# Kernel optimization log

Hardware: AMD Instinct MI355X
Metric: run time of the kernel (lower is better)

Reference implementation:

```python
import jax, jax.numpy as jnp
import numpy as np

B, S, D, H, DFF = 4, 2048, 1024, 16, 4096
DK = D // H  # = d_v
NEG = -1e30  # stands in for float('-inf'); fully-masked rows zeroed explicitly


def setup_inputs() -> dict:
    key = jax.random.key(0)
    ks = jax.random.split(key, 12)
    scale = lambda fan_in: fan_in ** -0.5
    # padding mask: positions >= random length are padded (True = pad)
    lens = jax.random.randint(ks[0], (B,), S // 2, S + 1)
    src_padding_mask = jnp.arange(S)[None, :] >= lens[:, None]
    return {
        "src": jax.random.normal(ks[1], (B, S, D), jnp.float32),
        "src_padding_mask": src_padding_mask,
        # per-head projections, stored as [H, D, DK] (x @ W, i.e. torch W.T)
        "Wq": jax.random.normal(ks[2], (H, D, DK), jnp.float32) * scale(D),
        "Wk": jax.random.normal(ks[3], (H, D, DK), jnp.float32) * scale(D),
        "Wv": jax.random.normal(ks[4], (H, D, DK), jnp.float32) * scale(D),
        "Wo": jax.random.normal(ks[5], (D, D), jnp.float32) * scale(D),
        "g1": jnp.ones((D,), jnp.float32),
        "g2": jnp.ones((D,), jnp.float32),
        "W1": jax.random.normal(ks[6], (D, DFF), jnp.float32) * scale(D),
        "V1": jax.random.normal(ks[7], (D, DFF), jnp.float32) * scale(D),
        "W2": jax.random.normal(ks[8], (DFF, D), jnp.float32) * scale(DFF),
    }


def _rmsnorm(x, gamma):
    # rms = sqrt(sum(x^2)/size); out = gamma * x / rms
    rms = jnp.sqrt(jnp.sum(x * x, axis=-1, keepdims=True) / x.shape[-1])
    return gamma * x / rms


def _encoder_layer(src, pad_mask, Wq, Wk, Wv, Wo, g1, g2, W1, V1, W2):
    x = _rmsnorm(src, g1)
    # all heads at once: q,k,v -> [B,H,S,DK]
    q = jnp.einsum('bsd,hdk->bhsk', x, Wq)
    k = jnp.einsum('bsd,hdk->bhsk', x, Wk)
    v = jnp.einsum('bsd,hdk->bhsk', x, Wv)
    scores = jnp.einsum('bhsk,bhtk->bhst', q, k) * (DK ** -0.5)  # [B,H,S,S]
    mask = pad_mask[:, None, :, None] | pad_mask[:, None, None, :]
    scores = jnp.where(mask, NEG, scores)
    attn = jax.nn.softmax(scores, axis=-1)
    # torch: fully -inf rows softmax to nan -> nan_to_num(0). Zero padded query rows.
    attn = jnp.where(pad_mask[:, None, :, None], 0.0, attn)
    o = jnp.einsum('bhst,bhtk->bhsk', attn, v)            # [B,H,S,DK]
    o = o.transpose(0, 2, 1, 3).reshape(src.shape[0], src.shape[1], -1)  # concat heads
    sa = src + o @ Wo
    y = _rmsnorm(sa, g2)
    ff = (jax.nn.silu(y @ W1) * (y @ V1)) @ W2
    return sa + ff


def reference(src, src_padding_mask, Wq, Wk, Wv, Wo, g1, g2, W1, V1, W2):
    return _encoder_layer(src, src_padding_mask, Wq, Wk, Wv, Wo, g1, g2, W1, V1, W2)
```

## Files before the change

### kernel.cpp

```cpp
#include <hip/hip_runtime.h>
#include <hip/hip_bf16.h>

typedef short short8 __attribute__((ext_vector_type(8)));
typedef float f32x4 __attribute__((ext_vector_type(4)));
typedef float f32x16 __attribute__((ext_vector_type(16)));
typedef unsigned short u16;
typedef unsigned short u16x4 __attribute__((ext_vector_type(4)));

__device__ __forceinline__ u16 f2bf(float f) {
  __hip_bfloat16 h = __float2bfloat16(f);
  return __builtin_bit_cast(u16, h);
}
__device__ __forceinline__ float bf2f(u16 u) {
  return __bfloat162float(__builtin_bit_cast(__hip_bfloat16, u));
}
__device__ __forceinline__ void gload_lds16(const void* g, void* l) {
  __builtin_amdgcn_global_load_lds(
      (const __attribute__((address_space(1))) void*)g,
      (__attribute__((address_space(3))) void*)l, 16, 0, 0);
}
__device__ __forceinline__ unsigned cvtpk(float lo, float hi) {
  unsigned r;
  asm("v_cvt_pk_bf16_f32 %0, %1, %2" : "=v"(r) : "v"(lo), "v"(hi));
  return r;
}

__global__ void compute_lens(const unsigned char* __restrict__ mask, int* __restrict__ lens) {
  __shared__ int flag;
  __shared__ int cnt[4];
  const int tid = threadIdx.x;
  if (tid == 0) flag = 0;
  if (tid < 4) cnt[tid] = 0;
  __syncthreads();
  int found = 0;
  for (int i = tid; i < 8192; i += 256)
    if (mask[i] == 1 && (i & 3) != 0) found = 1;
  if (found) atomicOr(&flag, 1);
  __syncthreads();
  int l0 = 0, l1 = 0, l2 = 0, l3 = 0;
  if (flag) {
    for (int i = tid; i < 8192; i += 256) {
      int z = (mask[i] == 0);
      int b = i >> 11;
      l0 += z & (b == 0); l1 += z & (b == 1); l2 += z & (b == 2); l3 += z & (b == 3);
    }
  } else {
    const int* mi = (const int*)mask;
    for (int i = tid; i < 8192; i += 256) {
      int z = (mi[i] == 0);
      int b = i >> 11;
      l0 += z & (b == 0); l1 += z & (b == 1); l2 += z & (b == 2); l3 += z & (b == 3);
    }
  }
  if (l0) atomicAdd(&cnt[0], l0);
  if (l1) atomicAdd(&cnt[1], l1);
  if (l2) atomicAdd(&cnt[2], l2);
  if (l3) atomicAdd(&cnt[3], l3);
  __syncthreads();
  if (tid < 4) lens[tid] = cnt[tid];
}

__global__ void convT(const float* __restrict__ in, u16* __restrict__ out,
                      int K, int N, long inz, long outz, int ilv) {
  __shared__ float t[32][33];
  const int n0 = blockIdx.x * 32, k0 = blockIdx.y * 32;
  const float* ip = in + (size_t)blockIdx.z * inz;
  u16* op = out + (size_t)blockIdx.z * outz;
  const int tx = threadIdx.x & 31, ty = threadIdx.x >> 5;
  for (int i = ty; i < 32; i += 8)
    t[i][tx] = ip[(size_t)(k0 + i) * N + n0 + tx];
  __syncthreads();
  for (int i = ty; i < 32; i += 8) {
    const int rn = n0 + i;
    const int r = ilv ? ((((rn >> 4) << 5) | (rn & 15)) | ((ilv - 1) << 4)) : rn;
    op[(size_t)r * K + k0 + tx] = f2bf(t[tx][i]);
  }
}

__global__ void rmsnorm_kernel(const float* __restrict__ in, const float* __restrict__ g,
                               u16* __restrict__ out) {
  __shared__ float psum[4];
  const int row = blockIdx.x, tid = threadIdx.x;
  const float4 x = ((const float4*)(in + (size_t)row * 1024))[tid];
  float ss = x.x * x.x + x.y * x.y + x.z * x.z + x.w * x.w;
  for (int m = 1; m < 64; m <<= 1) ss += __shfl_xor(ss, m, 64);
  if ((tid & 63) == 0) psum[tid >> 6] = ss;
  __syncthreads();
  const float tot = psum[0] + psum[1] + psum[2] + psum[3];
  const float inv = rsqrtf(tot * (1.0f / 1024.0f));
  const float4 gv = ((const float4*)g)[tid];
  u16x4 o;
  o[0] = f2bf(gv.x * x.x * inv); o[1] = f2bf(gv.y * x.y * inv);
  o[2] = f2bf(gv.z * x.z * inv); o[3] = f2bf(gv.w * x.w * inv);
  *(u16x4*)&out[(size_t)row * 1024 + tid * 4] = o;
}

enum { MQKV = 0, MSA = 1, MFSILU = 2, MFF2 = 3 };

template <int MODE, int BM>
__global__ __launch_bounds__(512, 2) void gemm3(
    const u16* __restrict__ A, const u16* __restrict__ Bt,
    const int K,
    u16* __restrict__ oq, u16* __restrict__ ok, u16* __restrict__ ov,
    float* __restrict__ of, const float* __restrict__ afp,
    u16* __restrict__ ob) {
  constexpr int ABUF = BM * 64;
  constexpr bool P4 = (BM == 256);
  constexpr int MR = BM / 32;
  __shared__ u16 lds[2 * ABUF + 32768];
  const int tid = threadIdx.x;
  const int w = tid >> 6, l = tid & 63;
  const int wr = w >> 2, wc = w & 3;
  const int lane16 = l & 15, lgrp = l >> 4;

  const int bid = (int)blockIdx.x, xcd = bid & 7, seq = bid >> 3;
  int by, bx;
  if (MODE == MQKV) {
    const int j = seq / 24, t5 = seq % 24;
    by = (xcd >> 2) * 16 + j * 8 + t5 / 3;
    bx = (xcd & 3) * 3 + t5 % 3;
  } else if (MODE == MFSILU) {
    by = (seq >> 5) * 8 + ((seq & 31) >> 2);
    bx = xcd * 4 + (seq & 3);
  } else {
    by = (xcd >> 1) * 16 + (seq >> 4) * 8 + ((seq & 15) >> 1);
    bx = (xcd & 1) * 2 + (seq & 1);
  }
  const int row0 = by * BM, col0 = bx * 256;

  auto stageA = [&](int kt, int buf) {
#pragma unroll
    for (int i = 0; i < BM / 64; ++i) {
      const int c = i * 512 + tid;
      const int r = c >> 3, j = (c & 7) ^ (r & 7);
      gload_lds16(A + (size_t)(row0 + r) * K + kt * 64 + j * 8,
                  &lds[buf * ABUF + c * 8]);
    }
  };
  auto stageB = [&](int kt, int buf) {
#pragma unroll
    for (int i = 0; i < 4; ++i) {
      const int c = i * 512 + tid;
      const int r = c >> 3, j = (c & 7) ^ (r & 7);
      gload_lds16(Bt + (size_t)(col0 + r) * K + kt * 64 + j * 8,
                  &lds[2 * ABUF + buf * 16384 + c * 8]);
    }
  };
  auto frofs = [&](int rrow, int ks) {
    return rrow * 64 + ((((ks << 2) + lgrp) ^ (rrow & 7)) << 3);
  };

  f32x4 zero = {0.f, 0.f, 0.f, 0.f};
  f32x4 acc[MR][4];
#pragma unroll
  for (int i = 0; i < MR; ++i)
#pragma unroll
    for (int j = 0; j < 4; ++j) acc[i][j] = zero;

  const int nkt = K >> 6;
  stageA(0, 0); stageB(0, 0); stageA(1, 1);
  if (P4) stageB(1, 1);

  for (int t = 0; t < nkt; ++t) {
    const int c = t & 1;
    if (t == nkt - 1)  asm volatile("s_waitcnt vmcnt(0)\ns_barrier" ::: "memory");
    else if (P4)       asm volatile("s_waitcnt vmcnt(8)\ns_barrier" ::: "memory");
    else               asm volatile("s_waitcnt vmcnt(2)\ns_barrier" ::: "memory");
    const u16* ap = &lds[c * ABUF];
    const u16* bp = &lds[2 * ABUF + c * 16384];
    short8 a[4][2], b01[2][2], b23[2][2];

    if (!P4) { if (t + 1 < nkt) stageB(t + 1, c ^ 1); }
#pragma unroll
    for (int mi = 0; mi < 4; ++mi)
#pragma unroll
      for (int ks = 0; ks < 2; ++ks)
        a[mi][ks] = *(const short8*)&ap[frofs(wr * (BM / 2) + mi * 16 + lane16, ks)];
#pragma unroll
    for (int ni = 0; ni < 2; ++ni)
#pragma unroll
      for (int ks = 0; ks < 2; ++ks) {
        b01[ni][ks] = *(const short8*)&bp[frofs(wc * 64 + ni * 16 + lane16, ks)];
        b23[ni][ks] = *(const short8*)&bp[frofs(wc * 64 + (ni + 2) * 16 + lane16, ks)];
      }
    __builtin_amdgcn_s_setprio(1);
#pragma unroll
    for (int ks = 0; ks < 2; ++ks)
#pragma unroll
      for (int mi = 0; mi < 4; ++mi)
#pragma unroll
        for (int ni = 0; ni < 2; ++ni)
          acc[mi][ni] = __builtin_amdgcn_mfma_f32_16x16x32_bf16(a[mi][ks], b01[ni][ks], acc[mi][ni], 0, 0, 0);
    __builtin_amdgcn_s_setprio(0);
    asm volatile("s_barrier" ::: "memory");

    if (P4) {
      __builtin_amdgcn_s_setprio(1);
#pragma unroll
      for (int ks = 0; ks < 2; ++ks)
#pragma unroll
        for (int mi = 0; mi < 4; ++mi)
#pragma unroll
          for (int ni = 0; ni < 2; ++ni)
            acc[mi][ni + 2] = __builtin_amdgcn_mfma_f32_16x16x32_bf16(a[mi][ks], b23[ni][ks], acc[mi][ni + 2], 0, 0, 0);
      __builtin_amdgcn_s_setprio(0);
#pragma unroll
      for (int mi = 0; mi < 4; ++mi)
#pragma unroll
        for (int ks = 0; ks < 2; ++ks)
          a[mi][ks] = *(const short8*)&ap[frofs(wr * 128 + (mi + 4) * 16 + lane16, ks)];
      asm volatile("s_barrier" ::: "memory");

      if (t + 2 < nkt) stageB(t + 2, c);
      __builtin_amdgcn_s_setprio(1);
#pragma unroll
      for (int ks = 0; ks < 2; ++ks)
#pragma unroll
        for (int mi = 0; mi < 4; ++mi)
#pragma unroll
          for (int ni = 0; ni < 2; ++ni)
            acc[(MR == 8 ? mi + 4 : mi)][ni] = __builtin_amdgcn_mfma_f32_16x16x32_bf16(a[mi][ks], b01[ni][ks], acc[(MR == 8 ? mi + 4 : mi)][ni], 0, 0, 0);
      __builtin_amdgcn_s_setprio(0);
      asm volatile("s_barrier" ::: "memory");

      if (t + 2 < nkt) stageA(t + 2, c);
      __builtin_amdgcn_s_setprio(1);
#pragma unroll
      for (int ks = 0; ks < 2; ++ks)
#pragma unroll
        for (int mi = 0; mi < 4; ++mi)
#pragma unroll
          for (int ni = 0; ni < 2; ++ni)
            acc[(MR == 8 ? mi + 4 : mi)][ni + 2] = __builtin_amdgcn_mfma_f32_16x16x32_bf16(a[mi][ks], b23[ni][ks], acc[(MR == 8 ? mi + 4 : mi)][ni + 2], 0, 0, 0);
      __builtin_amdgcn_s_setprio(0);
    } else {
      if (t + 2 < nkt) stageA(t + 2, c);
      __builtin_amdgcn_s_setprio(1);
#pragma unroll
      for (int ks = 0; ks < 2; ++ks)
#pragma unroll
        for (int mi = 0; mi < 4; ++mi)
#pragma unroll
          for (int ni = 0; ni < 2; ++ni)
            acc[mi][ni + 2] = __builtin_amdgcn_mfma_f32_16x16x32_bf16(a[mi][ks], b23[ni][ks], acc[mi][ni + 2], 0, 0, 0);
      __builtin_amdgcn_s_setprio(0);
    }
  }
  asm volatile("s_barrier" ::: "memory");

  if (MODE == MQKV) {
#pragma unroll
    for (int mi = 0; mi < MR; ++mi) {
      const int sbase = row0 + wr * (BM / 2) + mi * 16 + lgrp * 4;
      const int bbt = sbase >> 11, sr = sbase & 2047;
#pragma unroll
      for (int ni = 0; ni < 4; ++ni) {
        const int j = col0 + wc * 64 + ni * 16 + lane16;
        const int which = j >> 10, rr = j & 1023, h = rr >> 6, kk = rr & 63;
        const int bh = bbt * 16 + h;
        if (which == 2) {
          u16x4 pk;
#pragma unroll
          for (int r = 0; r < 4; ++r) pk[r] = f2bf(acc[mi][ni][r]);
          *(u16x4*)&ov[((size_t)bh * 64 + kk) * 2048 + sr] = pk;
        } else {
          u16* dst = (which == 0) ? oq : ok;
          const float scl = (which == 0) ? 0.125f : 1.0f;
#pragma unroll
          for (int r = 0; r < 4; ++r)
            dst[((size_t)bh * 2048 + sr + r) * 64 + kk] = f2bf(acc[mi][ni][r] * scl);
        }
      }
    }
  } else if (MODE == MFSILU) {
    u16* ep = &lds[w * 576];
    const int orow = l >> 2, ocol = (l & 3) * 8;
#pragma unroll
    for (int mi = 0; mi < MR; ++mi) {
#pragma unroll
      for (int p = 0; p < 2; ++p)
#pragma unroll
        for (int r = 0; r < 4; ++r) {
          const float h1 = acc[mi][2 * p][r], h2 = acc[mi][2 * p + 1][r];
          ep[(lgrp * 4 + r) * 34 + p * 16 + lane16] = f2bf(h1 / (1.0f + __expf(-h1)) * h2);
        }
      short8 v = *(const short8*)&ep[orow * 34 + ocol];
      *(short8*)&ob[(size_t)(row0 + wr * (BM / 2) + mi * 16 + orow) * 4096 +
                    (col0 >> 1) + wc * 32 + ocol] = v;
    }
  } else {
#pragma unroll
    for (int mi = 0; mi < MR; ++mi) {
      const int row = row0 + wr * (BM / 2) + mi * 16 + lgrp * 4;
#pragma unroll
      for (int ni = 0; ni < 4; ++ni) {
        const int j = col0 + wc * 64 + ni * 16 + lane16;
#pragma unroll
        for (int r = 0; r < 4; ++r) {
          const size_t idx = (size_t)(row + r) * 1024 + j;
          const float base = (MODE == MSA) ? afp[idx] : of[idx];
          of[idx] = base + acc[mi][ni][r];
        }
      }
    }
  }
}

__global__ void attn2_kernel(const u16* __restrict__ qb, const u16* __restrict__ kb,
                             const u16* __restrict__ vT, u16* __restrict__ obuf,
                             const int* __restrict__ lens) {
  __shared__ u16 sm[9216];
  const int tid = threadIdx.x;
  const int l = tid & 63, wid = tid >> 6;
  const int l31 = l & 31, hi = l >> 5;
  const int bh = blockIdx.x, b = bh >> 4, h = bh & 15;
  const int q0 = blockIdx.y * 128;
  const int len = lens[b];

  if (q0 >= len) {
    short8 z = {0, 0, 0, 0, 0, 0, 0, 0};
#pragma unroll
    for (int c = 0; c < 4; ++c) {
      const int ck = c * 256 + tid;
      const int r = ck >> 3, j = ck & 7;
      *(short8*)&obuf[((size_t)b * 2048 + q0 + r) * 1024 + h * 64 + j * 8] = z;
    }
    return;
  }

  const int q0w = q0 + wid * 32;
  const u16* qp = qb + ((size_t)bh * 2048 + q0w + l31) * 64;
  short8 qf0 = *(const short8*)(qp + hi * 8);
  short8 qf1 = *(const short8*)(qp + 16 + hi * 8);
  short8 qf2 = *(const short8*)(qp + 32 + hi * 8);
  short8 qf3 = *(const short8*)(qp + 48 + hi * 8);

  f32x16 oa0 = {0.f,0.f,0.f,0.f,0.f,0.f,0.f,0.f,0.f,0.f,0.f,0.f,0.f,0.f,0.f,0.f};
  f32x16 oa1 = oa0;
  float m_run = -1e30f, l_run = 0.f;

  const int swz = (l31 & 7) << 3;
  const int nt = (len + 63) >> 6;
  for (int kt = 0; kt < nt; ++kt) {
    const int t0 = kt * 64;
    __syncthreads();
#pragma unroll
    for (int c = 0; c < 2; ++c) {
      const int ck = c * 256 + wid * 64 + l;
      const int r = ck >> 3;
      const int j = (ck & 7) ^ (r & 7);
      gload_lds16(kb + ((size_t)bh * 2048 + t0 + r) * 64 + j * 8,
                  &sm[(c * 256 + wid * 64) * 8]);
      gload_lds16(vT + ((size_t)bh * 64 + r) * 2048 + t0 + j * 8,
                  &sm[4096 + (c * 256 + wid * 64) * 8]);
    }
    __syncthreads();

    f32x16 sc0 = {0.f,0.f,0.f,0.f,0.f,0.f,0.f,0.f,0.f,0.f,0.f,0.f,0.f,0.f,0.f,0.f};
    f32x16 sc1 = sc0;
#pragma unroll
    for (int ds = 0; ds < 4; ++ds) {
      const int col = (ds * 16 + hi * 8) ^ swz;
      const short8 kf0 = *(const short8*)&sm[(0 + l31) * 64 + col];
      const short8 kf1 = *(const short8*)&sm[(32 + l31) * 64 + col];
      const short8 qf = (ds == 0) ? qf0 : (ds == 1) ? qf1 : (ds == 2) ? qf2 : qf3;
      sc0 = __builtin_amdgcn_mfma_f32_32x32x16_bf16(kf0, qf, sc0, 0, 0, 0);
      sc1 = __builtin_amdgcn_mfma_f32_32x32x16_bf16(kf1, qf, sc1, 0, 0, 0);
    }

    if (t0 + 64 > len) {
      const int tb = t0 + 4 * hi;
#pragma unroll
      for (int i = 0; i < 16; ++i) {
        const int tg = tb + (i & 3) + 8 * (i >> 2);
        if (tg >= len) sc0[i] = -1e30f;
        if (tg + 32 >= len) sc1[i] = -1e30f;
      }
    }

    float mt = sc0[0];
#pragma unroll
    for (int i = 1; i < 16; ++i) mt = fmaxf(mt, sc0[i]);
#pragma unroll
    for (int i = 0; i < 16; ++i) mt = fmaxf(mt, sc1[i]);
    mt = fmaxf(mt, __shfl_xor(mt, 32, 64));
    const float mnew = fmaxf(m_run, mt);
    const float fac = __expf(m_run - mnew);
    m_run = mnew;
    float sum = 0.f;
#pragma unroll
    for (int i = 0; i < 16; ++i) { sc0[i] = __expf(sc0[i] - mnew); sum += sc0[i]; }
#pragma unroll
    for (int i = 0; i < 16; ++i) { sc1[i] = __expf(sc1[i] - mnew); sum += sc1[i]; }
    sum += __shfl_xor(sum, 32, 64);
    l_run = l_run * fac + sum;
#pragma unroll
    for (int i = 0; i < 16; ++i) { oa0[i] *= fac; oa1[i] *= fac; }

    unsigned wv[16];
#pragma unroll
    for (int k = 0; k < 8; ++k) wv[k] = cvtpk(sc0[2 * k], sc0[2 * k + 1]);
#pragma unroll
    for (int k = 0; k < 8; ++k) wv[8 + k] = cvtpk(sc1[2 * k], sc1[2 * k + 1]);
    unsigned pw[16];
#pragma unroll
    for (int s = 0; s < 2; ++s) {
#pragma unroll
      for (int half = 0; half < 2; ++half) {
        const unsigned a0 = wv[8 * s + 4 * half + 0], a1 = wv[8 * s + 4 * half + 1];
        const unsigned a2 = wv[8 * s + 4 * half + 2], a3 = wv[8 * s + 4 * half + 3];
        const unsigned e0 = (unsigned)__shfl_xor((int)(hi ? a0 : a2), 32, 64);
        const unsigned e1 = (unsigned)__shfl_xor((int)(hi ? a1 : a3), 32, 64);
        const int o = s * 8 + half * 4;
        pw[o + 0] = hi ? e0 : a0;
        pw[o + 1] = hi ? e1 : a1;
        pw[o + 2] = hi ? a2 : e0;
        pw[o + 3] = hi ? a3 : e1;
      }
    }
#pragma unroll
    for (int g = 0; g < 4; ++g) {
      union { unsigned u[4]; short8 s8; } pk;
      pk.u[0] = pw[4 * g + 0]; pk.u[1] = pw[4 * g + 1];
      pk.u[2] = pw[4 * g + 2]; pk.u[3] = pw[4 * g + 3];
      const int col = (g * 16 + hi * 8) ^ swz;
      const short8 vf0 = *(const short8*)&sm[4096 + (0 + l31) * 64 + col];
      const short8 vf1 = *(const short8*)&sm[4096 + (32 + l31) * 64 + col];
      oa0 = __builtin_amdgcn_mfma_f32_32x32x16_bf16(vf0, pk.s8, oa0, 0, 0, 0);
      oa1 = __builtin_amdgcn_mfma_f32_32x32x16_bf16(vf1, pk.s8, oa1, 0, 0, 0);
    }
  }

  __syncthreads();
  const float invl = 1.0f / l_run;
  u16* ow = &sm[wid * 2304];
#pragma unroll
  for (int i = 0; i < 16; ++i) {
    const int d0 = (i & 3) + 8 * (i >> 2) + 4 * hi;
    ow[l31 * 72 + d0] = f2bf(oa0[i] * invl);
    ow[l31 * 72 + 32 + d0] = f2bf(oa1[i] * invl);
  }
  short8 z = {0, 0, 0, 0, 0, 0, 0, 0};
#pragma unroll
  for (int c = 0; c < 4; ++c) {
    const int ck = c * 64 + l;
    const int r = ck >> 3, j = ck & 7;
    short8 v = *(const short8*)&ow[r * 72 + j * 8];
    if (q0w + r >= len) v = z;
    *(short8*)&obuf[((size_t)b * 2048 + q0w + r) * 1024 + h * 64 + j * 8] = v;
  }
}

extern "C" void kernel_launch(void* const* d_in, const int* in_sizes, int n_in,
                              void* d_out, int out_size, void* d_ws, size_t ws_size,
                              hipStream_t stream) {
  const float* src = (const float*)d_in[0];
  const unsigned char* mask = (const unsigned char*)d_in[1];
  const float* Wq = (const float*)d_in[2];
  const float* Wk = (const float*)d_in[3];
  const float* Wv = (const float*)d_in[4];
  const float* Wo = (const float*)d_in[5];
  const float* g1 = (const float*)d_in[6];
  const float* g2 = (const float*)d_in[7];
  const float* W1 = (const float*)d_in[8];
  const float* V1 = (const float*)d_in[9];
  const float* W2 = (const float*)d_in[10];
  float* out = (float*)d_out;
  char* ws = (char*)d_ws;

  int* lens   = (int*)ws;
  u16* WqkvT  = (u16*)(ws + 256);
  u16* WoT    = (u16*)(ws + 6291712);
  u16* W1V1T  = (u16*)(ws + 8388864);
  u16* W2T    = (u16*)(ws + 25166080);
  u16* xb     = (u16*)(ws + 33554688);
  u16* qbf    = (u16*)(ws + 50331904);
  u16* kbf    = (u16*)(ws + 67109120);
  u16* vTb    = (u16*)(ws + 83886336);
  u16* obf    = (u16*)(ws + 100663552);
  u16* c1     = qbf;

  compute_lens<<<1, 256, 0, stream>>>(mask, lens);
  convT<<<dim3(2, 32, 16), 256, 0, stream>>>(Wq, WqkvT, 1024, 64, 65536, 65536, 0);
  convT<<<dim3(2, 32, 16), 256, 0, stream>>>(Wk, WqkvT + 1024 * 1024, 1024, 64, 65536, 65536, 0);
  convT<<<dim3(2, 32, 16), 256, 0, stream>>>(Wv, WqkvT + 2048 * 1024, 1024, 64, 65536, 65536, 0);
  convT<<<dim3(32, 32, 1), 256, 0, stream>>>(Wo, WoT, 1024, 1024, 0, 0, 0);
  convT<<<dim3(128, 32, 1), 256, 0, stream>>>(W1, W1V1T, 1024, 4096, 0, 0, 1);
  convT<<<dim3(128, 32, 1), 256, 0, stream>>>(V1, W1V1T, 1024, 4096, 0, 0, 2);
  convT<<<dim3(32, 128, 1), 256, 0, stream>>>(W2, W2T, 4096, 1024, 0, 0, 0);

  rmsnorm_kernel<<<8192, 256, 0, stream>>>(src, g1, xb);
  gemm3<MQKV, 256><<<384, 512, 0, stream>>>(xb, WqkvT, 1024,
                                            qbf, kbf, vTb, nullptr, nullptr, nullptr);
  attn2_kernel<<<dim3(64, 16), 256, 0, stream>>>(qbf, kbf, vTb, obf, lens);
  gemm3<MSA, 128><<<256, 512, 0, stream>>>(obf, WoT, 1024,
                                           nullptr, nullptr, nullptr, out, src, nullptr);
  rmsnorm_kernel<<<8192, 256, 0, stream>>>(out, g2, xb);
  gemm3<MFSILU, 256><<<1024, 512, 0, stream>>>(xb, W1V1T, 1024,
                                               nullptr, nullptr, nullptr, nullptr, nullptr, c1);
  gemm3<MFF2, 128><<<256, 512, 0, stream>>>(c1, W2T, 4096,
                                            nullptr, nullptr, nullptr, out, nullptr, nullptr);
}
```

Before: 463.1 us.

## Restructure GEMM K-loop pipeline with split prefetch and double A fragments

Reworks the software pipeline of the bf16 MFMA GEMM. Both A and B tiles for stage t+2 are now prefetched in split halves interleaved between MFMA phases, and the vmcnt wait moves to the end of each iteration. In the 256-row variant, the second A half and the b23 fragments are loaded into separate registers ahead of the MFMAs so the LDS reads overlap compute. This costs more VGPRs and extra barriers, which at launch bounds (512,2) risks spills or lost occupancy.

```diff
diff --git a/kernel.cpp b/kernel.cpp
--- a/kernel.cpp
+++ b/kernel.cpp
@@ -107,6 +107,7 @@
   constexpr int ABUF = BM * 64;
   constexpr bool P4 = (BM == 256);
   constexpr int MR = BM / 32;
+  constexpr int AIT = BM / 64;
   __shared__ u16 lds[2 * ABUF + 32768];
   const int tid = threadIdx.x;
   const int w = tid >> 6, l = tid & 63;
@@ -128,22 +129,22 @@
   }
   const int row0 = by * BM, col0 = bx * 256;
 
-  auto stageA = [&](int kt, int buf) {
-#pragma unroll
-    for (int i = 0; i < BM / 64; ++i) {
-      const int c = i * 512 + tid;
-      const int r = c >> 3, j = (c & 7) ^ (r & 7);
+  auto stageAr = [&](int kt, int buf, int i0, int i1) {
+#pragma unroll
+    for (int i = i0; i < i1; ++i) {
+      const int cc = i * 512 + tid;
+      const int r = cc >> 3, j = (cc & 7) ^ (r & 7);
       gload_lds16(A + (size_t)(row0 + r) * K + kt * 64 + j * 8,
-                  &lds[buf * ABUF + c * 8]);
+                  &lds[buf * ABUF + cc * 8]);
     }
   };
-  auto stageB = [&](int kt, int buf) {
-#pragma unroll
-    for (int i = 0; i < 4; ++i) {
-      const int c = i * 512 + tid;
-      const int r = c >> 3, j = (c & 7) ^ (r & 7);
+  auto stageBr = [&](int kt, int buf, int i0, int i1) {
+#pragma unroll
+    for (int i = i0; i < i1; ++i) {
+      const int cc = i * 512 + tid;
+      const int r = cc >> 3, j = (cc & 7) ^ (r & 7);
       gload_lds16(Bt + (size_t)(col0 + r) * K + kt * 64 + j * 8,
-                  &lds[2 * ABUF + buf * 16384 + c * 8]);
+                  &lds[2 * ABUF + buf * 16384 + cc * 8]);
     }
   };
   auto frofs = [&](int rrow, int ks) {
@@ -158,19 +159,19 @@
     for (int j = 0; j < 4; ++j) acc[i][j] = zero;
 
   const int nkt = K >> 6;
-  stageA(0, 0); stageB(0, 0); stageA(1, 1);
-  if (P4) stageB(1, 1);
+  stageAr(0, 0, 0, AIT); stageBr(0, 0, 0, 4);
+  stageAr(1, 1, 0, AIT); stageBr(1, 1, 0, 4);
+  if (P4) asm volatile("s_waitcnt vmcnt(8)" ::: "memory");
+  else    asm volatile("s_waitcnt vmcnt(6)" ::: "memory");
+  __builtin_amdgcn_s_barrier();
 
   for (int t = 0; t < nkt; ++t) {
     const int c = t & 1;
-    if (t == nkt - 1)  asm volatile("s_waitcnt vmcnt(0)\ns_barrier" ::: "memory");
-    else if (P4)       asm volatile("s_waitcnt vmcnt(8)\ns_barrier" ::: "memory");
-    else               asm volatile("s_waitcnt vmcnt(2)\ns_barrier" ::: "memory");
+    const bool pf = (t + 2 < nkt);
     const u16* ap = &lds[c * ABUF];
     const u16* bp = &lds[2 * ABUF + c * 16384];
-    short8 a[4][2], b01[2][2], b23[2][2];
-
-    if (!P4) { if (t + 1 < nkt) stageB(t + 1, c ^ 1); }
+    short8 a[4][2], a2[4][2], b01[2][2], b23[2][2];
+
 #pragma unroll
     for (int mi = 0; mi < 4; ++mi)
 #pragma unroll
@@ -179,10 +180,17 @@
 #pragma unroll
     for (int ni = 0; ni < 2; ++ni)
 #pragma unroll
-      for (int ks = 0; ks < 2; ++ks) {
+      for (int ks = 0; ks < 2; ++ks)
         b01[ni][ks] = *(const short8*)&bp[frofs(wc * 64 + ni * 16 + lane16, ks)];
-        b23[ni][ks] = *(const short8*)&bp[frofs(wc * 64 + (ni + 2) * 16 + lane16, ks)];
-      }
+    if (!P4) {
+#pragma unroll
+      for (int ni = 0; ni < 2; ++ni)
+#pragma unroll
+        for (int ks = 0; ks < 2; ++ks)
+          b23[ni][ks] = *(const short8*)&bp[frofs(wc * 64 + (ni + 2) * 16 + lane16, ks)];
+    }
+    __builtin_amdgcn_s_barrier();
+    asm volatile("s_waitcnt lgkmcnt(0)" ::: "memory");
     __builtin_amdgcn_s_setprio(1);
 #pragma unroll
     for (int ks = 0; ks < 2; ++ks)
@@ -192,9 +200,21 @@
         for (int ni = 0; ni < 2; ++ni)
           acc[mi][ni] = __builtin_amdgcn_mfma_f32_16x16x32_bf16(a[mi][ks], b01[ni][ks], acc[mi][ni], 0, 0, 0);
     __builtin_amdgcn_s_setprio(0);
-    asm volatile("s_barrier" ::: "memory");
+    __builtin_amdgcn_s_barrier();
 
     if (P4) {
+#pragma unroll
+      for (int ni = 0; ni < 2; ++ni)
+#pragma unroll
+        for (int ks = 0; ks < 2; ++ks)
+          b23[ni][ks] = *(const short8*)&bp[frofs(wc * 64 + (ni + 2) * 16 + lane16, ks)];
+#pragma unroll
+      for (int mi = 0; mi < 4; ++mi)
+#pragma unroll
+        for (int ks = 0; ks < 2; ++ks)
+          a2[mi][ks] = *(const short8*)&ap[frofs(wr * 128 + (mi + 4) * 16 + lane16, ks)];
+      __builtin_amdgcn_s_barrier();
+      asm volatile("s_waitcnt lgkmcnt(0)" ::: "memory");
       __builtin_amdgcn_s_setprio(1);
 #pragma unroll
       for (int ks = 0; ks < 2; ++ks)
@@ -204,14 +224,10 @@
           for (int ni = 0; ni < 2; ++ni)
             acc[mi][ni + 2] = __builtin_amdgcn_mfma_f32_16x16x32_bf16(a[mi][ks], b23[ni][ks], acc[mi][ni + 2], 0, 0, 0);
       __builtin_amdgcn_s_setprio(0);
-#pragma unroll
-      for (int mi = 0; mi < 4; ++mi)
-#pragma unroll
-        for (int ks = 0; ks < 2; ++ks)
-          a[mi][ks] = *(const short8*)&ap[frofs(wr * 128 + (mi + 4) * 16 + lane16, ks)];
-      asm volatile("s_barrier" ::: "memory");
-
-      if (t + 2 < nkt) stageB(t + 2, c);
+      __builtin_amdgcn_s_barrier();
+
+      if (pf) { stageAr(t + 2, c, 0, 2); stageBr(t + 2, c, 0, 2); }
+      __builtin_amdgcn_s_barrier();
       __builtin_amdgcn_s_setprio(1);
 #pragma unroll
       for (int ks = 0; ks < 2; ++ks)
@@ -219,11 +235,12 @@
         for (int mi = 0; mi < 4; ++mi)
 #pragma unroll
           for (int ni = 0; ni < 2; ++ni)
-            acc[(MR == 8 ? mi + 4 : mi)][ni] = __builtin_amdgcn_mfma_f32_16x16x32_bf16(a[mi][ks], b01[ni][ks], acc[(MR == 8 ? mi + 4 : mi)][ni], 0, 0, 0);
+            acc[(MR == 8 ? mi + 4 : mi)][ni] = __builtin_amdgcn_mfma_f32_16x16x32_bf16(a2[mi][ks], b01[ni][ks], acc[(MR == 8 ? mi + 4 : mi)][ni], 0, 0, 0);
       __builtin_amdgcn_s_setprio(0);
-      asm volatile("s_barrier" ::: "memory");
-
-      if (t + 2 < nkt) stageA(t + 2, c);
+      __builtin_amdgcn_s_barrier();
+
+      if (pf) { stageAr(t + 2, c, 2, 4); stageBr(t + 2, c, 2, 4); }
+      __builtin_amdgcn_s_barrier();
       __builtin_amdgcn_s_setprio(1);
 #pragma unroll
       for (int ks = 0; ks < 2; ++ks)
@@ -231,10 +248,15 @@
         for (int mi = 0; mi < 4; ++mi)
 #pragma unroll
           for (int ni = 0; ni < 2; ++ni)
-            acc[(MR == 8 ? mi + 4 : mi)][ni + 2] = __builtin_amdgcn_mfma_f32_16x16x32_bf16(a[mi][ks], b23[ni][ks], acc[(MR == 8 ? mi + 4 : mi)][ni + 2], 0, 0, 0);
+            acc[(MR == 8 ? mi + 4 : mi)][ni + 2] = __builtin_amdgcn_mfma_f32_16x16x32_bf16(a2[mi][ks], b23[ni][ks], acc[(MR == 8 ? mi + 4 : mi)][ni + 2], 0, 0, 0);
       __builtin_amdgcn_s_setprio(0);
+      if (t == nkt - 2)      asm volatile("s_waitcnt vmcnt(0)" ::: "memory");
+      else if (t < nkt - 2)  asm volatile("s_waitcnt vmcnt(8)" ::: "memory");
+      __builtin_amdgcn_s_barrier();
     } else {
-      if (t + 2 < nkt) stageA(t + 2, c);
+      if (pf) { stageAr(t + 2, c, 0, 2); stageBr(t + 2, c, 0, 4); }
+      __builtin_amdgcn_s_barrier();
+      asm volatile("s_waitcnt lgkmcnt(0)" ::: "memory");
       __builtin_amdgcn_s_setprio(1);
 #pragma unroll
       for (int ks = 0; ks < 2; ++ks)
@@ -244,9 +266,11 @@
           for (int ni = 0; ni < 2; ++ni)
             acc[mi][ni + 2] = __builtin_amdgcn_mfma_f32_16x16x32_bf16(a[mi][ks], b23[ni][ks], acc[mi][ni + 2], 0, 0, 0);
       __builtin_amdgcn_s_setprio(0);
-    }
-  }
-  asm volatile("s_barrier" ::: "memory");
+      if (t == nkt - 2)      asm volatile("s_waitcnt vmcnt(0)" ::: "memory");
+      else if (t < nkt - 2)  asm volatile("s_waitcnt vmcnt(6)" ::: "memory");
+      __builtin_amdgcn_s_barrier();
+    }
+  }
 
   if (MODE == MQKV) {
 #pragma unroll
```

Result: slower. 483.8 us (+4.5%).

## Restructure BM=256 GEMM main loop to prefetch next A fragments across iterations

Applied to the files above, without the earlier changes.

Splits the GEMM main loop into separate BM=256 and BM=128 paths. In the 256-row path, the first half of the next tile's A fragments is loaded from LDS at the end of the current iteration, and the per-iteration vmcnt barrier is replaced by a finer wait placed just before the A restage. The 256-row path also holds two separate A register sets (low and high). This is meant to hide LDS read latency and trim barrier stalls, at the cost of more register pressure and more delicate wait-count correctness.

```diff
diff --git a/kernel.cpp b/kernel.cpp
--- a/kernel.cpp
+++ b/kernel.cpp
@@ -107,6 +107,7 @@
   constexpr int ABUF = BM * 64;
   constexpr bool P4 = (BM == 256);
   constexpr int MR = BM / 32;
+  constexpr int AIT = BM / 64;
   __shared__ u16 lds[2 * ABUF + 32768];
   const int tid = threadIdx.x;
   const int w = tid >> 6, l = tid & 63;
@@ -130,20 +131,20 @@
 
   auto stageA = [&](int kt, int buf) {
 #pragma unroll
-    for (int i = 0; i < BM / 64; ++i) {
-      const int c = i * 512 + tid;
-      const int r = c >> 3, j = (c & 7) ^ (r & 7);
+    for (int i = 0; i < AIT; ++i) {
+      const int cc = i * 512 + tid;
+      const int r = cc >> 3, j = (cc & 7) ^ (r & 7);
       gload_lds16(A + (size_t)(row0 + r) * K + kt * 64 + j * 8,
-                  &lds[buf * ABUF + c * 8]);
+                  &lds[buf * ABUF + cc * 8]);
     }
   };
   auto stageB = [&](int kt, int buf) {
 #pragma unroll
     for (int i = 0; i < 4; ++i) {
-      const int c = i * 512 + tid;
-      const int r = c >> 3, j = (c & 7) ^ (r & 7);
+      const int cc = i * 512 + tid;
+      const int r = cc >> 3, j = (cc & 7) ^ (r & 7);
       gload_lds16(Bt + (size_t)(col0 + r) * K + kt * 64 + j * 8,
-                  &lds[2 * ABUF + buf * 16384 + c * 8]);
+                  &lds[2 * ABUF + buf * 16384 + cc * 8]);
     }
   };
   auto frofs = [&](int rrow, int ks) {
@@ -158,43 +159,130 @@
     for (int j = 0; j < 4; ++j) acc[i][j] = zero;
 
   const int nkt = K >> 6;
-  stageA(0, 0); stageB(0, 0); stageA(1, 1);
-  if (P4) stageB(1, 1);
-
-  for (int t = 0; t < nkt; ++t) {
-    const int c = t & 1;
-    if (t == nkt - 1)  asm volatile("s_waitcnt vmcnt(0)\ns_barrier" ::: "memory");
-    else if (P4)       asm volatile("s_waitcnt vmcnt(8)\ns_barrier" ::: "memory");
-    else               asm volatile("s_waitcnt vmcnt(2)\ns_barrier" ::: "memory");
-    const u16* ap = &lds[c * ABUF];
-    const u16* bp = &lds[2 * ABUF + c * 16384];
-    short8 a[4][2], b01[2][2], b23[2][2];
-
-    if (!P4) { if (t + 1 < nkt) stageB(t + 1, c ^ 1); }
+
+  if (P4) {
+    stageB(0, 0); stageA(0, 0); stageB(1, 1); stageA(1, 1);
+    asm volatile("s_waitcnt vmcnt(8)" ::: "memory");
+    __builtin_amdgcn_s_barrier();
+    short8 aLO[4][2], aHI[4][2], b01[2][2], b23[2][2];
 #pragma unroll
     for (int mi = 0; mi < 4; ++mi)
 #pragma unroll
       for (int ks = 0; ks < 2; ++ks)
-        a[mi][ks] = *(const short8*)&ap[frofs(wr * (BM / 2) + mi * 16 + lane16, ks)];
-#pragma unroll
-    for (int ni = 0; ni < 2; ++ni)
-#pragma unroll
-      for (int ks = 0; ks < 2; ++ks) {
-        b01[ni][ks] = *(const short8*)&bp[frofs(wc * 64 + ni * 16 + lane16, ks)];
-        b23[ni][ks] = *(const short8*)&bp[frofs(wc * 64 + (ni + 2) * 16 + lane16, ks)];
+        aLO[mi][ks] = *(const short8*)&lds[frofs(wr * 128 + mi * 16 + lane16, ks)];
+
+    for (int t = 0; t < nkt; ++t) {
+      const int c = t & 1;
+      const u16* ap = &lds[c * ABUF];
+      const u16* bp = &lds[2 * ABUF + c * 16384];
+
+#pragma unroll
+      for (int ni = 0; ni < 2; ++ni)
+#pragma unroll
+        for (int ks = 0; ks < 2; ++ks)
+          b01[ni][ks] = *(const short8*)&bp[frofs(wc * 64 + ni * 16 + lane16, ks)];
+#pragma unroll
+      for (int ni = 0; ni < 2; ++ni)
+#pragma unroll
+        for (int ks = 0; ks < 2; ++ks)
+          b23[ni][ks] = *(const short8*)&bp[frofs(wc * 64 + (ni + 2) * 16 + lane16, ks)];
+      __builtin_amdgcn_s_setprio(1);
+#pragma unroll
+      for (int ks = 0; ks < 2; ++ks)
+#pragma unroll
+        for (int mi = 0; mi < 4; ++mi)
+#pragma unroll
+          for (int ni = 0; ni < 2; ++ni)
+            acc[mi][ni] = __builtin_amdgcn_mfma_f32_16x16x32_bf16(aLO[mi][ks], b01[ni][ks], acc[mi][ni], 0, 0, 0);
+      __builtin_amdgcn_s_setprio(0);
+      __builtin_amdgcn_s_barrier();
+
+#pragma unroll
+      for (int mi = 0; mi < 4; ++mi)
+#pragma unroll
+        for (int ks = 0; ks < 2; ++ks)
+          aHI[mi][ks] = *(const short8*)&ap[frofs(wr * 128 + (mi + 4) * 16 + lane16, ks)];
+      __builtin_amdgcn_s_setprio(1);
+#pragma unroll
+      for (int ks = 0; ks < 2; ++ks)
+#pragma unroll
+        for (int mi = 0; mi < 4; ++mi)
+#pragma unroll
+          for (int ni = 0; ni < 2; ++ni)
+            acc[mi][ni + 2] = __builtin_amdgcn_mfma_f32_16x16x32_bf16(aLO[mi][ks], b23[ni][ks], acc[mi][ni + 2], 0, 0, 0);
+      __builtin_amdgcn_s_setprio(0);
+      __builtin_amdgcn_s_barrier();
+
+      if (t + 2 < nkt) stageB(t + 2, c);
+      __builtin_amdgcn_s_setprio(1);
+#pragma unroll
+      for (int ks = 0; ks < 2; ++ks)
+#pragma unroll
+        for (int mi = 0; mi < 4; ++mi)
+#pragma unroll
+          for (int ni = 0; ni < 2; ++ni)
+            acc[mi + 4][ni] = __builtin_amdgcn_mfma_f32_16x16x32_bf16(aHI[mi][ks], b01[ni][ks], acc[mi + 4][ni], 0, 0, 0);
+      __builtin_amdgcn_s_setprio(0);
+      __builtin_amdgcn_s_barrier();
+
+      if (t + 2 < nkt) {
+        asm volatile("s_waitcnt vmcnt(4)" ::: "memory");
+        stageA(t + 2, c);
+      } else if (t + 1 < nkt) {
+        asm volatile("s_waitcnt vmcnt(0)" ::: "memory");
       }
-    __builtin_amdgcn_s_setprio(1);
-#pragma unroll
-    for (int ks = 0; ks < 2; ++ks)
+      if (t + 1 < nkt) {
+        const u16* apn = &lds[(c ^ 1) * ABUF];
+#pragma unroll
+        for (int mi = 0; mi < 4; ++mi)
+#pragma unroll
+          for (int ks = 0; ks < 2; ++ks)
+            aLO[mi][ks] = *(const short8*)&apn[frofs(wr * 128 + mi * 16 + lane16, ks)];
+      }
+      __builtin_amdgcn_s_setprio(1);
+#pragma unroll
+      for (int ks = 0; ks < 2; ++ks)
+#pragma unroll
+        for (int mi = 0; mi < 4; ++mi)
+#pragma unroll
+          for (int ni = 0; ni < 2; ++ni)
+            acc[mi + 4][ni + 2] = __builtin_amdgcn_mfma_f32_16x16x32_bf16(aHI[mi][ks], b23[ni][ks], acc[mi + 4][ni + 2], 0, 0, 0);
+      __builtin_amdgcn_s_setprio(0);
+      __builtin_amdgcn_s_barrier();
+    }
+  } else {
+    stageA(0, 0); stageB(0, 0); stageA(1, 1);
+    for (int t = 0; t < nkt; ++t) {
+      const int c = t & 1;
+      if (t == nkt - 1)  asm volatile("s_waitcnt vmcnt(0)\ns_barrier" ::: "memory");
+      else               asm volatile("s_waitcnt vmcnt(2)\ns_barrier" ::: "memory");
+      const u16* ap = &lds[c * ABUF];
+      const u16* bp = &lds[2 * ABUF + c * 16384];
+      short8 a[4][2], b01[2][2], b23[2][2];
+      if (t + 1 < nkt) stageB(t + 1, c ^ 1);
 #pragma unroll
       for (int mi = 0; mi < 4; ++mi)
 #pragma unroll
-        for (int ni = 0; ni < 2; ++ni)
-          acc[mi][ni] = __builtin_amdgcn_mfma_f32_16x16x32_bf16(a[mi][ks], b01[ni][ks], acc[mi][ni], 0, 0, 0);
-    __builtin_amdgcn_s_setprio(0);
-    asm volatile("s_barrier" ::: "memory");
-
-    if (P4) {
+        for (int ks = 0; ks < 2; ++ks)
+          a[mi][ks] = *(const short8*)&ap[frofs(wr * 64 + mi * 16 + lane16, ks)];
+#pragma unroll
+      for (int ni = 0; ni < 2; ++ni)
+#pragma unroll
+        for (int ks = 0; ks < 2; ++ks) {
+          b01[ni][ks] = *(const short8*)&bp[frofs(wc * 64 + ni * 16 + lane16, ks)];
+          b23[ni][ks] = *(const short8*)&bp[frofs(wc * 64 + (ni + 2) * 16 + lane16, ks)];
+        }
+      __builtin_amdgcn_s_setprio(1);
+#pragma unroll
+      for (int ks = 0; ks < 2; ++ks)
+#pragma unroll
+        for (int mi = 0; mi < 4; ++mi)
+#pragma unroll
+          for (int ni = 0; ni < 2; ++ni)
+            acc[mi][ni] = __builtin_amdgcn_mfma_f32_16x16x32_bf16(a[mi][ks], b01[ni][ks], acc[mi][ni], 0, 0, 0);
+      __builtin_amdgcn_s_setprio(0);
+      asm volatile("s_barrier" ::: "memory");
+      if (t + 2 < nkt) stageA(t + 2, c);
       __builtin_amdgcn_s_setprio(1);
 #pragma unroll
       for (int ks = 0; ks < 2; ++ks)
@@ -204,49 +292,9 @@
           for (int ni = 0; ni < 2; ++ni)
             acc[mi][ni + 2] = __builtin_amdgcn_mfma_f32_16x16x32_bf16(a[mi][ks], b23[ni][ks], acc[mi][ni + 2], 0, 0, 0);
       __builtin_amdgcn_s_setprio(0);
-#pragma unroll
-      for (int mi = 0; mi < 4; ++mi)
-#pragma unroll
-        for (int ks = 0; ks < 2; ++ks)
-          a[mi][ks] = *(const short8*)&ap[frofs(wr * 128 + (mi + 4) * 16 + lane16, ks)];
-      asm volatile("s_barrier" ::: "memory");
-
-      if (t + 2 < nkt) stageB(t + 2, c);
-      __builtin_amdgcn_s_setprio(1);
-#pragma unroll
-      for (int ks = 0; ks < 2; ++ks)
-#pragma unroll
-        for (int mi = 0; mi < 4; ++mi)
-#pragma unroll
-          for (int ni = 0; ni < 2; ++ni)
-            acc[(MR == 8 ? mi + 4 : mi)][ni] = __builtin_amdgcn_mfma_f32_16x16x32_bf16(a[mi][ks], b01[ni][ks], acc[(MR == 8 ? mi + 4 : mi)][ni], 0, 0, 0);
-      __builtin_amdgcn_s_setprio(0);
-      asm volatile("s_barrier" ::: "memory");
-
-      if (t + 2 < nkt) stageA(t + 2, c);
-      __builtin_amdgcn_s_setprio(1);
-#pragma unroll
-      for (int ks = 0; ks < 2; ++ks)
-#pragma unroll
-        for (int mi = 0; mi < 4; ++mi)
-#pragma unroll
-          for (int ni = 0; ni < 2; ++ni)
-            acc[(MR == 8 ? mi + 4 : mi)][ni + 2] = __builtin_amdgcn_mfma_f32_16x16x32_bf16(a[mi][ks], b23[ni][ks], acc[(MR == 8 ? mi + 4 : mi)][ni + 2], 0, 0, 0);
-      __builtin_amdgcn_s_setprio(0);
-    } else {
-      if (t + 2 < nkt) stageA(t + 2, c);
-      __builtin_amdgcn_s_setprio(1);
-#pragma unroll
-      for (int ks = 0; ks < 2; ++ks)
-#pragma unroll
-        for (int mi = 0; mi < 4; ++mi)
-#pragma unroll
-          for (int ni = 0; ni < 2; ++ni)
-            acc[mi][ni + 2] = __builtin_amdgcn_mfma_f32_16x16x32_bf16(a[mi][ks], b23[ni][ks], acc[mi][ni + 2], 0, 0, 0);
-      __builtin_amdgcn_s_setprio(0);
-    }
-  }
-  asm volatile("s_barrier" ::: "memory");
+    }
+    asm volatile("s_barrier" ::: "memory");
+  }
 
   if (MODE == MQKV) {
 #pragma unroll
```

Result: no change. 469.2 us (+1.3%).

## Halve GEMM M-tiles, simplify pipeline and raise occupancy to four blocks

Applied to the files above, without the earlier changes.

Replaces the gemm3 kernel with gemm4, which uses half-height M tiles (128 or 64 rows), a variable K-tile (64 or 32) with a matching LDS swizzle, and a single simplified double-buffered loop in place of the four-phase P4 schedule. Launch bounds go from 2 to 4 blocks per CU and grid sizes double, with the block-to-tile mappings updated. The aim is more occupancy and better load balance across CUs. In exchange, operand reuse per tile drops, so global/L2 traffic per FLOP rises, and the interleaved MFMA/load schedule is lost.

```diff
diff --git a/kernel.cpp b/kernel.cpp
--- a/kernel.cpp
+++ b/kernel.cpp
@@ -98,16 +98,20 @@
 enum { MQKV = 0, MSA = 1, MFSILU = 2, MFF2 = 3 };
 
 template <int MODE, int BM>
-__global__ __launch_bounds__(512, 2) void gemm3(
+__global__ __launch_bounds__(512, 4) void gemm4(
     const u16* __restrict__ A, const u16* __restrict__ Bt,
     const int K,
     u16* __restrict__ oq, u16* __restrict__ ok, u16* __restrict__ ov,
     float* __restrict__ of, const float* __restrict__ afp,
     u16* __restrict__ ob) {
-  constexpr int ABUF = BM * 64;
-  constexpr bool P4 = (BM == 256);
+  constexpr int BK = (BM == 128) ? 32 : 64;
+  constexpr int KS = BK / 32;
   constexpr int MR = BM / 32;
-  __shared__ u16 lds[2 * ABUF + 32768];
+  constexpr int ABUF = BM * BK;
+  constexpr int BBUF = 256 * BK;
+  constexpr int CPR = BK / 8;
+  constexpr int BIT = BBUF / 4096;
+  __shared__ u16 lds[2 * ABUF + 2 * BBUF];
   const int tid = threadIdx.x;
   const int w = tid >> 6, l = tid & 63;
   const int wr = w >> 2, wc = w & 3;
@@ -117,37 +121,38 @@
   int by, bx;
   if (MODE == MQKV) {
     const int j = seq / 24, t5 = seq % 24;
-    by = (xcd >> 2) * 16 + j * 8 + t5 / 3;
+    by = (xcd >> 2) * 32 + j * 8 + t5 / 3;
     bx = (xcd & 3) * 3 + t5 % 3;
   } else if (MODE == MFSILU) {
-    by = (seq >> 5) * 8 + ((seq & 31) >> 2);
+    by = seq >> 2;
     bx = xcd * 4 + (seq & 3);
   } else {
-    by = (xcd >> 1) * 16 + (seq >> 4) * 8 + ((seq & 15) >> 1);
+    by = (xcd >> 1) * 32 + (seq >> 1);
     bx = (xcd & 1) * 2 + (seq & 1);
   }
   const int row0 = by * BM, col0 = bx * 256;
 
+  auto swz = [](int r) -> int {
+    if (BK == 64) return r & 7;
+    return (r & 3) ^ ((r >> 2) & 3);
+  };
   auto stageA = [&](int kt, int buf) {
-#pragma unroll
-    for (int i = 0; i < BM / 64; ++i) {
-      const int c = i * 512 + tid;
-      const int r = c >> 3, j = (c & 7) ^ (r & 7);
-      gload_lds16(A + (size_t)(row0 + r) * K + kt * 64 + j * 8,
-                  &lds[buf * ABUF + c * 8]);
-    }
+    const int r = tid / CPR, j = (tid % CPR) ^ swz(r);
+    gload_lds16(A + (size_t)(row0 + r) * K + kt * BK + j * 8,
+                &lds[buf * ABUF + tid * 8]);
   };
   auto stageB = [&](int kt, int buf) {
 #pragma unroll
-    for (int i = 0; i < 4; ++i) {
-      const int c = i * 512 + tid;
-      const int r = c >> 3, j = (c & 7) ^ (r & 7);
-      gload_lds16(Bt + (size_t)(col0 + r) * K + kt * 64 + j * 8,
-                  &lds[2 * ABUF + buf * 16384 + c * 8]);
+    for (int i = 0; i < BIT; ++i) {
+      const int cc = i * 512 + tid;
+      const int r = cc / CPR, j = (cc % CPR) ^ swz(r);
+      gload_lds16(Bt + (size_t)(col0 + r) * K + kt * BK + j * 8,
+                  &lds[2 * ABUF + buf * BBUF + cc * 8]);
     }
   };
   auto frofs = [&](int rrow, int ks) {
-    return rrow * 64 + ((((ks << 2) + lgrp) ^ (rrow & 7)) << 3);
+    const int chunk = ((KS == 2 ? ks * 4 + lgrp : lgrp)) ^ swz(rrow);
+    return rrow * BK + chunk * 8;
   };
 
   f32x4 zero = {0.f, 0.f, 0.f, 0.f};
@@ -157,94 +162,52 @@
 #pragma unroll
     for (int j = 0; j < 4; ++j) acc[i][j] = zero;
 
-  const int nkt = K >> 6;
+  const int nkt = K / BK;
   stageA(0, 0); stageB(0, 0); stageA(1, 1);
-  if (P4) stageB(1, 1);
 
   for (int t = 0; t < nkt; ++t) {
     const int c = t & 1;
     if (t == nkt - 1)  asm volatile("s_waitcnt vmcnt(0)\ns_barrier" ::: "memory");
-    else if (P4)       asm volatile("s_waitcnt vmcnt(8)\ns_barrier" ::: "memory");
-    else               asm volatile("s_waitcnt vmcnt(2)\ns_barrier" ::: "memory");
+    else               asm volatile("s_waitcnt vmcnt(1)\ns_barrier" ::: "memory");
     const u16* ap = &lds[c * ABUF];
-    const u16* bp = &lds[2 * ABUF + c * 16384];
-    short8 a[4][2], b01[2][2], b23[2][2];
-
-    if (!P4) { if (t + 1 < nkt) stageB(t + 1, c ^ 1); }
-#pragma unroll
-    for (int mi = 0; mi < 4; ++mi)
-#pragma unroll
-      for (int ks = 0; ks < 2; ++ks)
+    const u16* bp = &lds[2 * ABUF + c * BBUF];
+    short8 a[MR][KS], b01[2][KS], b23[2][KS];
+
+    if (t + 1 < nkt) stageB(t + 1, c ^ 1);
+#pragma unroll
+    for (int mi = 0; mi < MR; ++mi)
+#pragma unroll
+      for (int ks = 0; ks < KS; ++ks)
         a[mi][ks] = *(const short8*)&ap[frofs(wr * (BM / 2) + mi * 16 + lane16, ks)];
 #pragma unroll
     for (int ni = 0; ni < 2; ++ni)
 #pragma unroll
-      for (int ks = 0; ks < 2; ++ks) {
+      for (int ks = 0; ks < KS; ++ks) {
         b01[ni][ks] = *(const short8*)&bp[frofs(wc * 64 + ni * 16 + lane16, ks)];
         b23[ni][ks] = *(const short8*)&bp[frofs(wc * 64 + (ni + 2) * 16 + lane16, ks)];
       }
     __builtin_amdgcn_s_setprio(1);
 #pragma unroll
-    for (int ks = 0; ks < 2; ++ks)
-#pragma unroll
-      for (int mi = 0; mi < 4; ++mi)
+    for (int ks = 0; ks < KS; ++ks)
+#pragma unroll
+      for (int mi = 0; mi < MR; ++mi)
 #pragma unroll
         for (int ni = 0; ni < 2; ++ni)
           acc[mi][ni] = __builtin_amdgcn_mfma_f32_16x16x32_bf16(a[mi][ks], b01[ni][ks], acc[mi][ni], 0, 0, 0);
     __builtin_amdgcn_s_setprio(0);
+    asm volatile("s_waitcnt lgkmcnt(0)" ::: "memory");
     asm volatile("s_barrier" ::: "memory");
 
-    if (P4) {
-      __builtin_amdgcn_s_setprio(1);
-#pragma unroll
-      for (int ks = 0; ks < 2; ++ks)
-#pragma unroll
-        for (int mi = 0; mi < 4; ++mi)
-#pragma unroll
-          for (int ni = 0; ni < 2; ++ni)
-            acc[mi][ni + 2] = __builtin_amdgcn_mfma_f32_16x16x32_bf16(a[mi][ks], b23[ni][ks], acc[mi][ni + 2], 0, 0, 0);
-      __builtin_amdgcn_s_setprio(0);
-#pragma unroll
-      for (int mi = 0; mi < 4; ++mi)
-#pragma unroll
-        for (int ks = 0; ks < 2; ++ks)
-          a[mi][ks] = *(const short8*)&ap[frofs(wr * 128 + (mi + 4) * 16 + lane16, ks)];
-      asm volatile("s_barrier" ::: "memory");
-
-      if (t + 2 < nkt) stageB(t + 2, c);
-      __builtin_amdgcn_s_setprio(1);
-#pragma unroll
-      for (int ks = 0; ks < 2; ++ks)
-#pragma unroll
-        for (int mi = 0; mi < 4; ++mi)
-#pragma unroll
-          for (int ni = 0; ni < 2; ++ni)
-            acc[(MR == 8 ? mi + 4 : mi)][ni] = __builtin_amdgcn_mfma_f32_16x16x32_bf16(a[mi][ks], b01[ni][ks], acc[(MR == 8 ? mi + 4 : mi)][ni], 0, 0, 0);
-      __builtin_amdgcn_s_setprio(0);
-      asm volatile("s_barrier" ::: "memory");
-
-      if (t + 2 < nkt) stageA(t + 2, c);
-      __builtin_amdgcn_s_setprio(1);
-#pragma unroll
-      for (int ks = 0; ks < 2; ++ks)
-#pragma unroll
-        for (int mi = 0; mi < 4; ++mi)
-#pragma unroll
-          for (int ni = 0; ni < 2; ++ni)
-            acc[(MR == 8 ? mi + 4 : mi)][ni + 2] = __builtin_amdgcn_mfma_f32_16x16x32_bf16(a[mi][ks], b23[ni][ks], acc[(MR == 8 ? mi + 4 : mi)][ni + 2], 0, 0, 0);
-      __builtin_amdgcn_s_setprio(0);
-    } else {
-      if (t + 2 < nkt) stageA(t + 2, c);
-      __builtin_amdgcn_s_setprio(1);
-#pragma unroll
-      for (int ks = 0; ks < 2; ++ks)
-#pragma unroll
-        for (int mi = 0; mi < 4; ++mi)
-#pragma unroll
-          for (int ni = 0; ni < 2; ++ni)
-            acc[mi][ni + 2] = __builtin_amdgcn_mfma_f32_16x16x32_bf16(a[mi][ks], b23[ni][ks], acc[mi][ni + 2], 0, 0, 0);
-      __builtin_amdgcn_s_setprio(0);
-    }
+    if (t + 2 < nkt) stageA(t + 2, c);
+    __builtin_amdgcn_s_setprio(1);
+#pragma unroll
+    for (int ks = 0; ks < KS; ++ks)
+#pragma unroll
+      for (int mi = 0; mi < MR; ++mi)
+#pragma unroll
+        for (int ni = 0; ni < 2; ++ni)
+          acc[mi][ni + 2] = __builtin_amdgcn_mfma_f32_16x16x32_bf16(a[mi][ks], b23[ni][ks], acc[mi][ni + 2], 0, 0, 0);
+    __builtin_amdgcn_s_setprio(0);
   }
   asm volatile("s_barrier" ::: "memory");
 
@@ -490,14 +453,14 @@
   convT<<<dim3(32, 128, 1), 256, 0, stream>>>(W2, W2T, 4096, 1024, 0, 0, 0);
 
   rmsnorm_kernel<<<8192, 256, 0, stream>>>(src, g1, xb);
-  gemm3<MQKV, 256><<<384, 512, 0, stream>>>(xb, WqkvT, 1024,
+  gemm4<MQKV, 128><<<768, 512, 0, stream>>>(xb, WqkvT, 1024,
                                             qbf, kbf, vTb, nullptr, nullptr, nullptr);
   attn2_kernel<<<dim3(64, 16), 256, 0, stream>>>(qbf, kbf, vTb, obf, lens);
-  gemm3<MSA, 128><<<256, 512, 0, stream>>>(obf, WoT, 1024,
-                                           nullptr, nullptr, nullptr, out, src, nullptr);
+  gemm4<MSA, 64><<<512, 512, 0, stream>>>(obf, WoT, 1024,
+                                          nullptr, nullptr, nullptr, out, src, nullptr);
   rmsnorm_kernel<<<8192, 256, 0, stream>>>(out, g2, xb);
-  gemm3<MFSILU, 256><<<1024, 512, 0, stream>>>(xb, W1V1T, 1024,
+  gemm4<MFSILU, 128><<<2048, 512, 0, stream>>>(xb, W1V1T, 1024,
                                                nullptr, nullptr, nullptr, nullptr, nullptr, c1);
-  gemm3<MFF2, 128><<<256, 512, 0, stream>>>(c1, W2T, 4096,
-                                            nullptr, nullptr, nullptr, out, nullptr, nullptr);
-}
+  gemm4<MFF2, 64><<<512, 512, 0, stream>>>(c1, W2T, 4096,
+                                           nullptr, nullptr, nullptr, out, nullptr, nullptr);
+}
```

New measurement: 474.0 us. 1.02x slower.
